# Performance work log

Measured on AMD Instinct MI355X. Metric: run time of the kernel, lower is better.

Reference implementation:

```python
import jax, jax.numpy as jnp
import numpy as np

HEADS = 4
DIM_HEAD = 32
EPS = 1e-5


def setup_inputs() -> dict:
    key = jax.random.key(0)
    ks = jax.random.split(key, 3)
    b, c, h, w = 32, 256, 64, 64
    hidden = HEADS * DIM_HEAD  # 128
    x = jax.random.normal(ks[0], (b, c, h, w), dtype=jnp.float32)
    w_qkv = jax.random.normal(ks[1], (3 * hidden, c), dtype=jnp.float32) * 0.02
    w_out = jax.random.normal(ks[2], (c, hidden), dtype=jnp.float32) * 0.02
    b_out = jnp.zeros((c,), dtype=jnp.float32)
    gn_w = jnp.ones((c,), dtype=jnp.float32)
    gn_b = jnp.zeros((c,), dtype=jnp.float32)
    return {"x": x, "w_qkv": w_qkv, "w_out": w_out, "b_out": b_out,
            "gn_w": gn_w, "gn_b": gn_b}


def reference(x, w_qkv, w_out, b_out, gn_w, gn_b):
    b, c, h, w = x.shape
    n = h * w
    scale = DIM_HEAD ** (-0.5)
    # 1x1 conv (no bias) -> qkv, shape (b, 3*hidden, h, w)
    qkv = jnp.einsum('bchw,oc->bohw', x, w_qkv)
    qkv = qkv.reshape(b, 3, HEADS, DIM_HEAD, n)
    q, k, v = qkv[:, 0], qkv[:, 1], qkv[:, 2]  # each (b, H, d, n)
    q = jax.nn.softmax(q, axis=-2) * scale     # softmax over d
    k = jax.nn.softmax(k, axis=-1)             # softmax over n
    # linear attention core
    context = jnp.einsum('bhdn,bhen->bhde', k, v)   # (b, H, d, e)
    out = jnp.einsum('bhde,bhdn->bhen', context, q)  # (b, H, e, n)
    out = out.reshape(b, HEADS * DIM_HEAD, h, w)
    # 1x1 conv with bias
    out = jnp.einsum('bchw,oc->bohw', out, w_out) + b_out[None, :, None, None]
    # GroupNorm(1, dim): normalize over (C, H, W) per sample
    mean = out.mean(axis=(1, 2, 3), keepdims=True)
    var = out.var(axis=(1, 2, 3), keepdims=True)
    out = (out - mean) * jax.lax.rsqrt(var + EPS)
    out = out * gn_w[None, :, None, None] + gn_b[None, :, None, None]
    return out
```

## Files before the change

### kernel.cpp

```cpp
#include <hip/hip_runtime.h>
#include <math.h>

#define B_ 32
#define C_ 256
#define N_ 4096
#define HID_ 128
#define OC3_ 384
#define HEADS_ 4
#define DH_ 32
#define LNM_ (C_*N_)
#define CTXP_ 4

typedef unsigned short u16;
typedef __attribute__((ext_vector_type(8))) short short8;
typedef __attribute__((ext_vector_type(4))) float f32x4;

__device__ inline u16 f2b(float f) {
  union { float f; unsigned int u; } c; c.f = f;
  unsigned int u = c.u;
  return (u16)((u + 0x7fffu + ((u >> 16) & 1u)) >> 16);
}
__device__ inline float b2f(u16 b) {
  union { float f; unsigned int u; } c; c.u = (unsigned int)b << 16; return c.f;
}
__device__ inline void load_lds16(const u16* g, u16* l) {
  __builtin_amdgcn_global_load_lds(
      (const __attribute__((address_space(1))) void*)g,
      (__attribute__((address_space(3))) void*)l, 16, 0, 0);
}

__global__ void k_cast_w(const float* __restrict__ wq, const float* __restrict__ wo,
                         u16* __restrict__ wqb, u16* __restrict__ wob,
                         float* __restrict__ bsum) {
  int i = blockIdx.x * 256 + threadIdx.x;
  if (i < OC3_ * C_) wqb[i] = f2b(wq[i]);
  if (i < C_ * HID_) wob[i] = f2b(wo[i]);
  if (i < 64) bsum[i] = 0.f;
}

__global__ __launch_bounds__(256) void k_transpose(const float* __restrict__ x,
                                                   u16* __restrict__ xt) {
  int b = blockIdx.z;
  int n0 = blockIdx.x * 64, c0 = blockIdx.y * 64;
  __shared__ float t[64][65];
  const float* xp = x + (size_t)b * C_ * N_;
  u16* xo = xt + (size_t)b * N_ * C_;
  int tid = threadIdx.x;
  int r = tid >> 4, c4 = (tid & 15) * 4;
  #pragma unroll
  for (int i = 0; i < 4; i++) {
    int cl = r + i * 16;
    float4 v = *(const float4*)&xp[(size_t)(c0 + cl) * N_ + n0 + c4];
    t[cl][c4 + 0] = v.x; t[cl][c4 + 1] = v.y; t[cl][c4 + 2] = v.z; t[cl][c4 + 3] = v.w;
  }
  __syncthreads();
  #pragma unroll
  for (int i = 0; i < 4; i++) {
    int nl = r + i * 16;
    ushort4 o;
    o.x = f2b(t[c4 + 0][nl]); o.y = f2b(t[c4 + 1][nl]);
    o.z = f2b(t[c4 + 2][nl]); o.w = f2b(t[c4 + 3][nl]);
    *(ushort4*)&xo[(size_t)(n0 + nl) * C_ + c0 + c4] = o;
  }
}

template<int KDIM, bool OUTBF16>
__global__ __launch_bounds__(256) void k_gemm_mfma(
    const u16* __restrict__ A, const u16* __restrict__ Ball, void* __restrict__ Call,
    const float* __restrict__ bias, float* __restrict__ bsum, int Mtot) {
  int b = blockIdx.z;
  int m0 = blockIdx.y * 128, n0 = blockIdx.x * 128;
  const u16* Bt = Ball + (size_t)b * N_ * KDIM;
  __shared__ __align__(16) u16 As[4096];
  __shared__ __align__(16) u16 Bs[4096];
  __shared__ float red[8];
  int tid = threadIdx.x;
  int w = tid >> 6, l = tid & 63, l16 = l & 15, quad = l >> 4;
  int wm = w & 1, wn = w >> 1;
  f32x4 acc[4][4] = {};

  for (int k0 = 0; k0 < KDIM; k0 += 32) {
    #pragma unroll
    for (int i = 0; i < 2; i++) {
      int chunk = i * 256 + tid;
      int c = chunk >> 7, m = chunk & 127;
      const u16* ga = A  + (size_t)(m0 + m) * KDIM + k0 + c * 8;
      const u16* gb = Bt + (size_t)(n0 + m) * KDIM + k0 + c * 8;
      u16* la = As + (size_t)(i * 256 + (tid & ~63)) * 8;
      u16* lb = Bs + (size_t)(i * 256 + (tid & ~63)) * 8;
      load_lds16(ga, la);
      load_lds16(gb, lb);
    }
    __syncthreads();
    short8 af[4], bf[4];
    #pragma unroll
    for (int mi = 0; mi < 4; mi++)
      af[mi] = *(const short8*)&As[(size_t)(quad * 128 + wm * 64 + mi * 16 + l16) * 8];
    #pragma unroll
    for (int nj = 0; nj < 4; nj++)
      bf[nj] = *(const short8*)&Bs[(size_t)(quad * 128 + wn * 64 + nj * 16 + l16) * 8];
    #pragma unroll
    for (int mi = 0; mi < 4; mi++)
      #pragma unroll
      for (int nj = 0; nj < 4; nj++)
        acc[mi][nj] = __builtin_amdgcn_mfma_f32_16x16x32_bf16(af[mi], bf[nj], acc[mi][nj], 0, 0, 0);
    __syncthreads();
  }

  if constexpr (OUTBF16) {
    u16* Co = (u16*)Call + (size_t)b * Mtot * N_;
    u16* lw = As + w * 1024;
    #pragma unroll
    for (int mi = 0; mi < 4; mi++) {
      #pragma unroll
      for (int nj = 0; nj < 4; nj++)
        #pragma unroll
        for (int r = 0; r < 4; r++)
          lw[(quad * 4 + r) * 64 + nj * 16 + l16] = f2b(acc[mi][nj][r]);
      #pragma unroll
      for (int p = 0; p < 2; p++) {
        int chunk = p * 64 + l;
        int row = chunk >> 3, cc = chunk & 7;
        uint4 v = *(const uint4*)&lw[chunk * 8];
        *(uint4*)&Co[(size_t)(m0 + wm * 64 + mi * 16 + row) * N_ + n0 + wn * 64 + cc * 8] = v;
      }
    }
  } else {
    float* Co = (float*)Call + (size_t)b * Mtot * N_;
    float s1 = 0.f, s2 = 0.f;
    #pragma unroll
    for (int mi = 0; mi < 4; mi++)
      #pragma unroll
      for (int r = 0; r < 4; r++) {
        int m = m0 + wm * 64 + mi * 16 + quad * 4 + r;
        float bv = bias[m];
        #pragma unroll
        for (int nj = 0; nj < 4; nj++) {
          int n = n0 + wn * 64 + nj * 16 + l16;
          float v = acc[mi][nj][r] + bv;
          s1 += v; s2 += v * v;
          Co[(size_t)m * N_ + n] = v;
        }
      }
    #pragma unroll
    for (int o = 32; o; o >>= 1) { s1 += __shfl_xor(s1, o); s2 += __shfl_xor(s2, o); }
    if (l == 0) { red[w] = s1; red[4 + w] = s2; }
    __syncthreads();
    if (tid == 0) {
      atomicAdd(&bsum[2 * b],     red[0] + red[1] + red[2] + red[3]);
      atomicAdd(&bsum[2 * b + 1], red[4] + red[5] + red[6] + red[7]);
    }
  }
}

__global__ __launch_bounds__(256) void k_kstats(const u16* __restrict__ qkvb,
    float* __restrict__ rmax, float* __restrict__ rinv) {
  int r = blockIdx.x;
  int b = r >> 7, rem = r & 127;
  const u16* row = qkvb + (size_t)b * OC3_ * N_ + (size_t)(HID_ + rem) * N_;
  int tid = threadIdx.x;
  float v[16];
  #pragma unroll
  for (int p = 0; p < 2; p++) {
    uint4 u = *(const uint4*)&row[(size_t)(p * 256 + tid) * 8];
    unsigned int uu[4] = {u.x, u.y, u.z, u.w};
    #pragma unroll
    for (int j = 0; j < 4; j++) {
      v[p * 8 + j * 2 + 0] = b2f((u16)(uu[j] & 0xffff));
      v[p * 8 + j * 2 + 1] = b2f((u16)(uu[j] >> 16));
    }
  }
  float m = -1e30f;
  #pragma unroll
  for (int i = 0; i < 16; i++) m = fmaxf(m, v[i]);
  #pragma unroll
  for (int o = 32; o; o >>= 1) m = fmaxf(m, __shfl_xor(m, o));
  __shared__ float sm[4], ss[4];
  int w = tid >> 6;
  if ((tid & 63) == 0) sm[w] = m;
  __syncthreads();
  m = fmaxf(fmaxf(sm[0], sm[1]), fmaxf(sm[2], sm[3]));
  float s = 0.f;
  #pragma unroll
  for (int i = 0; i < 16; i++) s += __expf(v[i] - m);
  #pragma unroll
  for (int o = 32; o; o >>= 1) s += __shfl_xor(s, o);
  if ((tid & 63) == 0) ss[w] = s;
  __syncthreads();
  if (tid == 0) {
    rmax[r] = m;
    rinv[r] = 1.f / (ss[0] + ss[1] + ss[2] + ss[3]);
  }
}

__global__ __launch_bounds__(256) void k_context(const u16* __restrict__ qkvb,
    const float* __restrict__ rmax, const float* __restrict__ rinv,
    float* __restrict__ ctxp) {
  int blk = blockIdx.x, bh = blockIdx.y;
  int b = bh >> 2, hd = bh & 3;
  const u16* kb = qkvb + (size_t)b * OC3_ * N_ + (size_t)(HID_ + hd * DH_) * N_;
  const u16* vb = qkvb + (size_t)b * OC3_ * N_ + (size_t)(2 * HID_ + hd * DH_) * N_;
  __shared__ float redl[4096];
  int tid = threadIdx.x;
  int w = tid >> 6, l = tid & 63, l16 = l & 15, quad = l >> 4;
  float rm[2], ri[2];
  #pragma unroll
  for (int mi = 0; mi < 2; mi++) {
    rm[mi] = rmax[bh * 32 + mi * 16 + l16];
    ri[mi] = rinv[bh * 32 + mi * 16 + l16];
  }
  f32x4 acc[2][2] = {};
  int nbase = blk * 1024 + w * 256 + quad * 8;
  #pragma unroll
  for (int kk = 0; kk < 8; kk++) {
    int n0 = nbase + kk * 32;
    short8 af[2], bf[2];
    #pragma unroll
    for (int nj = 0; nj < 2; nj++)
      bf[nj] = *(const short8*)&vb[(size_t)(nj * 16 + l16) * N_ + n0];
    #pragma unroll
    for (int mi = 0; mi < 2; mi++) {
      uint4 u = *(const uint4*)&kb[(size_t)(mi * 16 + l16) * N_ + n0];
      unsigned int uu[4] = {u.x, u.y, u.z, u.w};
      union { unsigned int u[4]; short8 s; } pk;
      #pragma unroll
      for (int j = 0; j < 4; j++) {
        float lo = __expf(b2f((u16)(uu[j] & 0xffff)) - rm[mi]) * ri[mi];
        float hi = __expf(b2f((u16)(uu[j] >> 16))     - rm[mi]) * ri[mi];
        pk.u[j] = (unsigned int)f2b(lo) | ((unsigned int)f2b(hi) << 16);
      }
      af[mi] = pk.s;
    }
    #pragma unroll
    for (int mi = 0; mi < 2; mi++)
      #pragma unroll
      for (int nj = 0; nj < 2; nj++)
        acc[mi][nj] = __builtin_amdgcn_mfma_f32_16x16x32_bf16(af[mi], bf[nj], acc[mi][nj], 0, 0, 0);
  }
  #pragma unroll
  for (int mi = 0; mi < 2; mi++)
    #pragma unroll
    for (int nj = 0; nj < 2; nj++)
      #pragma unroll
      for (int r = 0; r < 4; r++)
        redl[w * 1024 + (mi * 16 + quad * 4 + r) * 32 + nj * 16 + l16] = acc[mi][nj][r];
  __syncthreads();
  float* cp = ctxp + (size_t)blk * 131072 + (size_t)bh * 1024;
  #pragma unroll
  for (int j = 0; j < 4; j++) {
    int idx = j * 256 + tid;
    cp[idx] = redl[idx] + redl[1024 + idx] + redl[2048 + idx] + redl[3072 + idx];
  }
}

__global__ __launch_bounds__(256) void k_attnout(const u16* __restrict__ qkvb,
    const float* __restrict__ ctxp, u16* __restrict__ hidt) {
  int tile = blockIdx.x, bh = blockIdx.y;
  int b = bh >> 2, hd = bh & 3;
  const u16* qbase = qkvb + (size_t)b * OC3_ * N_ + (size_t)(hd * DH_) * N_;
  __shared__ float cs[32][40];
  __shared__ unsigned int hs[256][16];
  int tid = threadIdx.x;
  for (int idx = tid; idx < 1024; idx += 256) {
    float s = 0.f;
    #pragma unroll
    for (int p = 0; p < CTXP_; p++)
      s += ctxp[(size_t)p * 131072 + (size_t)bh * 1024 + idx];
    int d = idx >> 5, e = idx & 31;
    cs[d][e] = s;
  }
  __syncthreads();
  int n = tile * 256 + tid;
  float q[32];
  float m = -1e30f;
  #pragma unroll
  for (int d = 0; d < 32; d++) { q[d] = b2f(qbase[(size_t)d * N_ + n]); m = fmaxf(m, q[d]); }
  float s = 0.f;
  #pragma unroll
  for (int d = 0; d < 32; d++) { q[d] = __expf(q[d] - m); s += q[d]; }
  float inv = 0.17677669529663687f / s;
  #pragma unroll
  for (int d = 0; d < 32; d++) q[d] *= inv;
  #pragma unroll
  for (int e0 = 0; e0 < 32; e0 += 4) {
    f32x4 a = {};
    #pragma unroll
    for (int d = 0; d < 32; d++) {
      f32x4 c4 = *(const f32x4*)&cs[d][e0];
      a += q[d] * c4;
    }
    hs[tid][e0 / 2 + 0] = (unsigned int)f2b(a[0]) | ((unsigned int)f2b(a[1]) << 16);
    hs[tid][e0 / 2 + 1] = (unsigned int)f2b(a[2]) | ((unsigned int)f2b(a[3]) << 16);
  }
  __syncthreads();
  #pragma unroll
  for (int it = 0; it < 8; it++) {
    int q2 = it * 256 + tid;
    int nl = q2 >> 3, c2 = q2 & 7;
    uint2 v = *(const uint2*)&hs[nl][c2 * 2];
    *(uint2*)&hidt[((size_t)b * N_ + tile * 256 + nl) * HID_ + hd * 32 + c2 * 4] = v;
  }
}

__global__ void k_finalize(float* __restrict__ bsum) {
  int b = threadIdx.x;
  if (b < B_) {
    float s1 = bsum[2 * b], s2 = bsum[2 * b + 1];
    float mean = s1 * (1.f / LNM_);
    float var = s2 * (1.f / LNM_) - mean * mean;
    bsum[2 * b] = mean;
    bsum[2 * b + 1] = rsqrtf(var + 1e-5f);
  }
}

__global__ __launch_bounds__(256) void k_norm(float* __restrict__ out,
    const float* __restrict__ bsum, const float* __restrict__ gnw,
    const float* __restrict__ gnb) {
  size_t v = (size_t)blockIdx.x * 256 + threadIdx.x;
  int c = (int)((v >> 10) & 255);
  int b = (int)(v >> 18);
  float mean = bsum[2 * b], rstd = bsum[2 * b + 1];
  float w = gnw[c] * rstd;
  float sh = gnb[c] - mean * w;
  float4 x = ((const float4*)out)[v];
  x.x = x.x * w + sh; x.y = x.y * w + sh;
  x.z = x.z * w + sh; x.w = x.w * w + sh;
  ((float4*)out)[v] = x;
}

extern "C" void kernel_launch(void* const* d_in, const int* in_sizes, int n_in,
                              void* d_out, int out_size, void* d_ws, size_t ws_size,
                              hipStream_t stream) {
  const float* x     = (const float*)d_in[0];
  const float* w_qkv = (const float*)d_in[1];
  const float* w_out = (const float*)d_in[2];
  const float* b_out = (const float*)d_in[3];
  const float* gn_w  = (const float*)d_in[4];
  const float* gn_b  = (const float*)d_in[5];
  float* out = (float*)d_out;

  u16* qkvb = (u16*)d_ws;
  u16* xt   = qkvb + (size_t)B_ * OC3_ * N_;
  u16* hidt = xt;
  float* ctx  = (float*)(xt + (size_t)B_ * N_ * C_);
  float* bsum = ctx + CTXP_ * 131072;
  float* rmax = bsum + 64;
  float* rinv = rmax + 4096;
  u16* wqb = (u16*)(rinv + 4096);
  u16* wob = wqb + OC3_ * C_;

  k_cast_w<<<384, 256, 0, stream>>>(w_qkv, w_out, wqb, wob, bsum);
  k_transpose<<<dim3(64, 4, 32), 256, 0, stream>>>(x, xt);
  k_gemm_mfma<256, true><<<dim3(32, 3, 32), 256, 0, stream>>>(wqb, xt, qkvb, nullptr, nullptr, OC3_);
  k_kstats<<<4096, 256, 0, stream>>>(qkvb, rmax, rinv);
  k_context<<<dim3(CTXP_, 128), 256, 0, stream>>>(qkvb, rmax, rinv, ctx);
  k_attnout<<<dim3(16, 128), 256, 0, stream>>>(qkvb, ctx, hidt);
  k_gemm_mfma<128, false><<<dim3(32, 2, 32), 256, 0, stream>>>(wob, hidt, out, b_out, bsum, C_);
  k_finalize<<<1, 64, 0, stream>>>(bsum);
  k_norm<<<32768, 256, 0, stream>>>(out, bsum, gn_w, gn_b);
}
```

Measured before the change: 454.4 us.

## Fuse input transpose and weight cast into the MFMA GEMM loaders

Removes the separate weight-cast and x-transpose kernels. The GEMMs now read fp32 weights directly and convert them to bf16 while staging into LDS. The first GEMM also reads x in its native channel-major layout, converting and transposing in registers before writing the B tile to LDS. This drops a full read and write of x plus two launches, in exchange for synchronous (non-async) loads with in-loop conversions, and redundant weight conversion across every block; bsum zeroing moves into k_kstats.

```diff
diff --git a/kernel.cpp b/kernel.cpp
--- a/kernel.cpp
+++ b/kernel.cpp
@@ -29,48 +29,13 @@
       (__attribute__((address_space(3))) void*)l, 16, 0, 0);
 }
 
-__global__ void k_cast_w(const float* __restrict__ wq, const float* __restrict__ wo,
-                         u16* __restrict__ wqb, u16* __restrict__ wob,
-                         float* __restrict__ bsum) {
-  int i = blockIdx.x * 256 + threadIdx.x;
-  if (i < OC3_ * C_) wqb[i] = f2b(wq[i]);
-  if (i < C_ * HID_) wob[i] = f2b(wo[i]);
-  if (i < 64) bsum[i] = 0.f;
-}
-
-__global__ __launch_bounds__(256) void k_transpose(const float* __restrict__ x,
-                                                   u16* __restrict__ xt) {
-  int b = blockIdx.z;
-  int n0 = blockIdx.x * 64, c0 = blockIdx.y * 64;
-  __shared__ float t[64][65];
-  const float* xp = x + (size_t)b * C_ * N_;
-  u16* xo = xt + (size_t)b * N_ * C_;
-  int tid = threadIdx.x;
-  int r = tid >> 4, c4 = (tid & 15) * 4;
-  #pragma unroll
-  for (int i = 0; i < 4; i++) {
-    int cl = r + i * 16;
-    float4 v = *(const float4*)&xp[(size_t)(c0 + cl) * N_ + n0 + c4];
-    t[cl][c4 + 0] = v.x; t[cl][c4 + 1] = v.y; t[cl][c4 + 2] = v.z; t[cl][c4 + 3] = v.w;
-  }
-  __syncthreads();
-  #pragma unroll
-  for (int i = 0; i < 4; i++) {
-    int nl = r + i * 16;
-    ushort4 o;
-    o.x = f2b(t[c4 + 0][nl]); o.y = f2b(t[c4 + 1][nl]);
-    o.z = f2b(t[c4 + 2][nl]); o.w = f2b(t[c4 + 3][nl]);
-    *(ushort4*)&xo[(size_t)(n0 + nl) * C_ + c0 + c4] = o;
-  }
-}
-
-template<int KDIM, bool OUTBF16>
+template<int KDIM, bool OUTBF16, bool BFUSED>
 __global__ __launch_bounds__(256) void k_gemm_mfma(
-    const u16* __restrict__ A, const u16* __restrict__ Ball, void* __restrict__ Call,
+    const float* __restrict__ Af, const u16* __restrict__ Ball,
+    const float* __restrict__ Xall, void* __restrict__ Call,
     const float* __restrict__ bias, float* __restrict__ bsum, int Mtot) {
   int b = blockIdx.z;
   int m0 = blockIdx.y * 128, n0 = blockIdx.x * 128;
-  const u16* Bt = Ball + (size_t)b * N_ * KDIM;
   __shared__ __align__(16) u16 As[4096];
   __shared__ __align__(16) u16 Bs[4096];
   __shared__ float red[8];
@@ -79,17 +44,45 @@
   int wm = w & 1, wn = w >> 1;
   f32x4 acc[4][4] = {};
 
+  const u16* Bt = BFUSED ? nullptr : (Ball + (size_t)b * N_ * KDIM);
+  const float* Xb = BFUSED ? (Xall + (size_t)b * KDIM * N_) : nullptr;
+
   for (int k0 = 0; k0 < KDIM; k0 += 32) {
-    #pragma unroll
-    for (int i = 0; i < 2; i++) {
-      int chunk = i * 256 + tid;
-      int c = chunk >> 7, m = chunk & 127;
-      const u16* ga = A  + (size_t)(m0 + m) * KDIM + k0 + c * 8;
-      const u16* gb = Bt + (size_t)(n0 + m) * KDIM + k0 + c * 8;
-      u16* la = As + (size_t)(i * 256 + (tid & ~63)) * 8;
-      u16* lb = Bs + (size_t)(i * 256 + (tid & ~63)) * 8;
-      load_lds16(ga, la);
-      load_lds16(gb, lb);
+    {
+      int m = tid & 127, kh = tid >> 7;
+      const float* ga = Af + (size_t)(m0 + m) * KDIM + k0 + kh * 16;
+      float4 v0 = *(const float4*)(ga + 0);
+      float4 v1 = *(const float4*)(ga + 4);
+      float4 v2 = *(const float4*)(ga + 8);
+      float4 v3 = *(const float4*)(ga + 12);
+      union { u16 h[8]; uint4 q; } p0, p1;
+      p0.h[0] = f2b(v0.x); p0.h[1] = f2b(v0.y); p0.h[2] = f2b(v0.z); p0.h[3] = f2b(v0.w);
+      p0.h[4] = f2b(v1.x); p0.h[5] = f2b(v1.y); p0.h[6] = f2b(v1.z); p0.h[7] = f2b(v1.w);
+      p1.h[0] = f2b(v2.x); p1.h[1] = f2b(v2.y); p1.h[2] = f2b(v2.z); p1.h[3] = f2b(v2.w);
+      p1.h[4] = f2b(v3.x); p1.h[5] = f2b(v3.y); p1.h[6] = f2b(v3.z); p1.h[7] = f2b(v3.w);
+      *(uint4*)&As[(size_t)(kh * 2 + 0) * 1024 + m * 8] = p0.q;
+      *(uint4*)&As[(size_t)(kh * 2 + 1) * 1024 + m * 8] = p1.q;
+    }
+    if constexpr (BFUSED) {
+      int nl = (tid & 63) * 2, cb = tid >> 6;
+      const float* gb = Xb + (size_t)(k0 + cb * 8) * N_ + n0 + nl;
+      float2 e[8];
+      #pragma unroll
+      for (int ci = 0; ci < 8; ci++) e[ci] = *(const float2*)(gb + (size_t)ci * N_);
+      union { u16 h[8]; uint4 q; } lo, hi;
+      #pragma unroll
+      for (int ci = 0; ci < 8; ci++) { lo.h[ci] = f2b(e[ci].x); hi.h[ci] = f2b(e[ci].y); }
+      *(uint4*)&Bs[(size_t)cb * 1024 + (nl + 0) * 8] = lo.q;
+      *(uint4*)&Bs[(size_t)cb * 1024 + (nl + 1) * 8] = hi.q;
+    } else {
+      #pragma unroll
+      for (int i = 0; i < 2; i++) {
+        int chunk = i * 256 + tid;
+        int c = chunk >> 7, m = chunk & 127;
+        const u16* gb = Bt + (size_t)(n0 + m) * KDIM + k0 + c * 8;
+        u16* lb = Bs + (size_t)(i * 256 + (tid & ~63)) * 8;
+        load_lds16(gb, lb);
+      }
     }
     __syncthreads();
     short8 af[4], bf[4];
@@ -154,11 +147,12 @@
 }
 
 __global__ __launch_bounds__(256) void k_kstats(const u16* __restrict__ qkvb,
-    float* __restrict__ rmax, float* __restrict__ rinv) {
+    float* __restrict__ rmax, float* __restrict__ rinv, float* __restrict__ bsum) {
   int r = blockIdx.x;
   int b = r >> 7, rem = r & 127;
   const u16* row = qkvb + (size_t)b * OC3_ * N_ + (size_t)(HID_ + rem) * N_;
   int tid = threadIdx.x;
+  if (r == 0 && tid < 64) bsum[tid] = 0.f;
   float v[16];
   #pragma unroll
   for (int p = 0; p < 2; p++) {
@@ -340,22 +334,19 @@
   float* out = (float*)d_out;
 
   u16* qkvb = (u16*)d_ws;
-  u16* xt   = qkvb + (size_t)B_ * OC3_ * N_;
-  u16* hidt = xt;
-  float* ctx  = (float*)(xt + (size_t)B_ * N_ * C_);
+  u16* hidt = qkvb + (size_t)B_ * OC3_ * N_;
+  float* ctx  = (float*)(hidt + (size_t)B_ * N_ * HID_);
   float* bsum = ctx + CTXP_ * 131072;
   float* rmax = bsum + 64;
   float* rinv = rmax + 4096;
-  u16* wqb = (u16*)(rinv + 4096);
-  u16* wob = wqb + OC3_ * C_;
-
-  k_cast_w<<<384, 256, 0, stream>>>(w_qkv, w_out, wqb, wob, bsum);
-  k_transpose<<<dim3(64, 4, 32), 256, 0, stream>>>(x, xt);
-  k_gemm_mfma<256, true><<<dim3(32, 3, 32), 256, 0, stream>>>(wqb, xt, qkvb, nullptr, nullptr, OC3_);
-  k_kstats<<<4096, 256, 0, stream>>>(qkvb, rmax, rinv);
+
+  k_gemm_mfma<256, true, true><<<dim3(32, 3, 32), 256, 0, stream>>>(
+      w_qkv, nullptr, x, qkvb, nullptr, nullptr, OC3_);
+  k_kstats<<<4096, 256, 0, stream>>>(qkvb, rmax, rinv, bsum);
   k_context<<<dim3(CTXP_, 128), 256, 0, stream>>>(qkvb, rmax, rinv, ctx);
   k_attnout<<<dim3(16, 128), 256, 0, stream>>>(qkvb, ctx, hidt);
-  k_gemm_mfma<128, false><<<dim3(32, 2, 32), 256, 0, stream>>>(wob, hidt, out, b_out, bsum, C_);
+  k_gemm_mfma<128, false, false><<<dim3(32, 2, 32), 256, 0, stream>>>(
+      w_out, hidt, nullptr, out, b_out, bsum, C_);
   k_finalize<<<1, 64, 0, stream>>>(bsum);
   k_norm<<<32768, 256, 0, stream>>>(out, bsum, gn_w, gn_b);
 }
```

Result: faster. 443.1 us (-2.5%).
